# Kernel tuning notes

Hardware: AMD Instinct MI355X
Metric: run time of the kernel (lower is better)

The kernel has to match this reference:

```python
import jax, jax.numpy as jnp
import numpy as np

N = 50000      # nodes
E = 600000     # edges (avg degree 12)
IN, H, OUT = 128, 256, 256


def setup_inputs() -> dict:
    key = jax.random.key(0)
    ks = jax.random.split(key, 9)
    glorot = lambda k, shp: jax.random.uniform(
        k, shp, jnp.float32, -1.0, 1.0) * np.sqrt(6.0 / (shp[0] + shp[1]))
    return {
        "x": jax.random.normal(ks[0], (N, IN), jnp.float32),
        "src": jax.random.randint(ks[1], (E,), 0, N, jnp.int32),
        "dst": jax.random.randint(ks[2], (E,), 0, N, jnp.int32),
        "W_conv": glorot(ks[3], (IN, H)),
        "b_conv": jnp.zeros((H,), jnp.float32),
        "W_fc": glorot(ks[4], (H, H)),
        "b_fc": jax.random.uniform(ks[5], (H,), jnp.float32, -1, 1) / np.sqrt(H),
        "W_fc2": glorot(ks[6], (H, OUT)),
        "b_fc2": jax.random.uniform(ks[7], (OUT,), jnp.float32, -1, 1) / np.sqrt(OUT),
    }


def reference(x, src, dst, W_conv, b_conv, W_fc, b_fc, W_fc2, b_fc2):
    ones = jnp.ones((E,), x.dtype)
    # dgl GraphConv, norm='both': D_in^{-1/2} A D_out^{-1/2} X W + b
    deg_out = jax.ops.segment_sum(ones, src, num_segments=N)
    deg_in = jax.ops.segment_sum(ones, dst, num_segments=N)
    norm_src = jax.lax.rsqrt(jnp.maximum(deg_out, 1.0))  # [N]
    norm_dst = jax.lax.rsqrt(jnp.maximum(deg_in, 1.0))   # [N]
    feat = x * norm_src[:, None]                          # [N, IN]
    agg = jax.ops.segment_sum(feat[src], dst, num_segments=N)  # gather+scatter SpMM
    h = agg * norm_dst[:, None]
    h = h @ W_conv + b_conv                               # GraphConv weight+bias
    # num_nonl_layers == 2 branch
    h = jax.nn.relu(h) @ W_fc + b_fc
    h = jax.nn.relu(h) @ W_fc2 + b_fc2
    return h
```

## Files before the change

kernel.cpp:

```cpp
#include <hip/hip_runtime.h>

#define NN 50000
#define NE 600000
#define FIN 128
#define CAPS 128
#define CAPU 64
#define PW1 136
#define PW2 264

typedef __attribute__((ext_vector_type(8))) short bf16x8;
typedef __attribute__((ext_vector_type(4))) float f32x4;

__device__ __forceinline__ unsigned short f2bf(float f) {
    union { float f; unsigned int i; } v; v.f = f;
    return (unsigned short)((v.i + 0x7FFFu + ((v.i >> 16) & 1u)) >> 16);
}


__global__ __launch_bounds__(256)
void bin_kernel(const int* __restrict__ src, const int* __restrict__ dst,
                int* __restrict__ cnt_in, int* __restrict__ cnt_out,
                int* __restrict__ csr_src) {
    int e = blockIdx.x * 256 + threadIdx.x;
    if (e < NE) {
        int s = src[e], d = dst[e];
        int p = atomicAdd(&cnt_in[d], 1);
        if (p < CAPU) csr_src[d * CAPS + p] = s;
        atomicAdd(&cnt_out[s], 1);
    }
}

__global__ __launch_bounds__(256)
void gather_kernel(const float* __restrict__ x, const int* __restrict__ csr_src,
                   const int* __restrict__ cnt_in, const int* __restrict__ cnt_out,
                   char* __restrict__ slotbase) {
    int tid  = threadIdx.x;
    int grp  = tid >> 5;
    int lane = tid & 31;
    int r = blockIdx.x * 8 + grp;
    if (r >= NN) return;
    int deg = cnt_in[r];
    float nd = rsqrtf(fmaxf((float)deg, 1.0f));
    int cnt = deg > CAPU ? CAPU : deg;
    const int* bucket = csr_src + (size_t)r * CAPS;
    const float* xb = x + lane * 4;
    float4 acc = {0.f, 0.f, 0.f, 0.f};
    for (int j0 = 0; j0 < cnt; j0 += 32) {
        int c = cnt - j0; if (c > 32) c = 32;
        int sv = 0; float nsl = 0.f;
        if (lane < c) {
            sv  = bucket[j0 + lane];
            nsl = rsqrtf(fmaxf((float)cnt_out[sv], 1.0f));
        }
        int i = 0;
        for (; i + 4 <= c; i += 4) {
            int   s0 = __shfl(sv, i, 32),     s1 = __shfl(sv, i + 1, 32);
            int   s2 = __shfl(sv, i + 2, 32), s3 = __shfl(sv, i + 3, 32);
            float n0 = __shfl(nsl, i, 32),     n1 = __shfl(nsl, i + 1, 32);
            float n2 = __shfl(nsl, i + 2, 32), n3 = __shfl(nsl, i + 3, 32);
            float4 v0 = *(const float4*)(xb + (size_t)s0 * FIN);
            float4 v1 = *(const float4*)(xb + (size_t)s1 * FIN);
            float4 v2 = *(const float4*)(xb + (size_t)s2 * FIN);
            float4 v3 = *(const float4*)(xb + (size_t)s3 * FIN);
            acc.x += v0.x * n0; acc.y += v0.y * n0; acc.z += v0.z * n0; acc.w += v0.w * n0;
            acc.x += v1.x * n1; acc.y += v1.y * n1; acc.z += v1.z * n1; acc.w += v1.w * n1;
            acc.x += v2.x * n2; acc.y += v2.y * n2; acc.z += v2.z * n2; acc.w += v2.w * n2;
            acc.x += v3.x * n3; acc.y += v3.y * n3; acc.z += v3.z * n3; acc.w += v3.w * n3;
        }
        for (; i < c; ++i) {
            int   s  = __shfl(sv,  i, 32);
            float ns = __shfl(nsl, i, 32);
            float4 xv = *(const float4*)(xb + (size_t)s * FIN);
            acc.x += xv.x * ns; acc.y += xv.y * ns;
            acc.z += xv.z * ns; acc.w += xv.w * ns;
        }
    }
    unsigned short o[4];
    o[0] = f2bf(acc.x * nd); o[1] = f2bf(acc.y * nd);
    o[2] = f2bf(acc.z * nd); o[3] = f2bf(acc.w * nd);
    *(uint2*)(slotbase + (size_t)r * 1024 + 768 + lane * 8) = *(const uint2*)o;
}

__global__ __launch_bounds__(256)
void wprep_kernel(const float* __restrict__ Wc, const float* __restrict__ W1,
                  const float* __restrict__ W2, unsigned short* __restrict__ o) {
    int t = blockIdx.x * 256 + threadIdx.x;
    if (t < 32768) {
        int n = t >> 7, k = t & 127;
        o[t] = f2bf(Wc[k * 256 + n]);
    } else if (t < 98304) {
        int i = t - 32768; int n = i >> 8, k = i & 255;
        o[32768 + i] = f2bf(W1[k * 256 + n]);
    } else if (t < 163840) {
        int i = t - 98304; int n = i >> 8, k = i & 255;
        o[98304 + i] = f2bf(W2[k * 256 + n]);
    }
}

__global__ __launch_bounds__(256)
void gemm1_kernel(char* slotbase, const unsigned short* __restrict__ Wct,
                  const float* __restrict__ bc) {
    __shared__ short wsh[64 * PW1];
    int tid = threadIdx.x;
    int wave = tid >> 6, lane = tid & 63;
    int quad = lane >> 4, l16 = lane & 15;
    int m0 = blockIdx.x * 128 + wave * 32;
    bf16x8 a[2][4];
    #pragma unroll
    for (int g = 0; g < 2; ++g) {
        int arow = m0 + g * 16 + l16; if (arow >= NN) arow = NN - 1;
        const unsigned short* Ap =
            (const unsigned short*)(slotbase + (size_t)arow * 1024 + 768) + quad * 8;
        #pragma unroll
        for (int i = 0; i < 4; ++i) a[g][i] = *(const bf16x8*)(Ap + i * 32);
    }
    int sc = tid >> 2, sq = tid & 3;
    #pragma unroll 1
    for (int p = 0; p < 4; ++p) {
        __syncthreads();
        {
            const unsigned short* g = Wct + (size_t)(p * 64 + sc) * 128 + sq * 32;
            #pragma unroll
            for (int j = 0; j < 4; ++j)
                *(bf16x8*)&wsh[sc * PW1 + sq * 32 + j * 8] = *(const bf16x8*)(g + j * 8);
        }
        __syncthreads();
        f32x4 acc[2][4] = {};
        #pragma unroll
        for (int i = 0; i < 4; ++i) {
            int k0 = i * 32;
            bf16x8 b0 = *(const bf16x8*)&wsh[( 0 + l16) * PW1 + quad * 8 + k0];
            bf16x8 b1 = *(const bf16x8*)&wsh[(16 + l16) * PW1 + quad * 8 + k0];
            bf16x8 b2 = *(const bf16x8*)&wsh[(32 + l16) * PW1 + quad * 8 + k0];
            bf16x8 b3 = *(const bf16x8*)&wsh[(48 + l16) * PW1 + quad * 8 + k0];
            #pragma unroll
            for (int g = 0; g < 2; ++g) {
                acc[g][0] = __builtin_amdgcn_mfma_f32_16x16x32_bf16(a[g][i], b0, acc[g][0], 0, 0, 0);
                acc[g][1] = __builtin_amdgcn_mfma_f32_16x16x32_bf16(a[g][i], b1, acc[g][1], 0, 0, 0);
                acc[g][2] = __builtin_amdgcn_mfma_f32_16x16x32_bf16(a[g][i], b2, acc[g][2], 0, 0, 0);
                acc[g][3] = __builtin_amdgcn_mfma_f32_16x16x32_bf16(a[g][i], b3, acc[g][3], 0, 0, 0);
            }
        }
        int n0 = p * 64;
        #pragma unroll
        for (int c = 0; c < 4; ++c) {
            int col = n0 + c * 16 + l16;
            float bv = bc[col];
            #pragma unroll
            for (int g = 0; g < 2; ++g) {
                #pragma unroll
                for (int r2 = 0; r2 < 4; ++r2) {
                    int rr = m0 + g * 16 + quad * 4 + r2;
                    if (rr < NN)
                        *(unsigned short*)(slotbase + (size_t)rr * 1024 + 512 + 2 * col) =
                            f2bf(fmaxf(acc[g][c][r2] + bv, 0.0f));
                }
            }
        }
    }
}

template<bool FINAL>
__global__ __launch_bounds__(256)
void gemm23_kernel(char* slotbase, const unsigned short* __restrict__ Wt,
                   const float* __restrict__ bias) {
    __shared__ short wsh[64 * PW2];
    int tid = threadIdx.x;
    int wave = tid >> 6, lane = tid & 63;
    int quad = lane >> 4, l16 = lane & 15;
    int m0 = blockIdx.x * 128 + wave * 32;
    bf16x8 a[2][8];
    #pragma unroll
    for (int g = 0; g < 2; ++g) {
        int arow = m0 + g * 16 + l16; if (arow >= NN) arow = NN - 1;
        const unsigned short* Ap =
            (const unsigned short*)(slotbase + (size_t)arow * 1024 + (FINAL ? 0 : 512)) + quad * 8;
        #pragma unroll
        for (int i = 0; i < 8; ++i) a[g][i] = *(const bf16x8*)(Ap + i * 32);
    }
    int sc = tid >> 2, sq = tid & 3;
    #pragma unroll 1
    for (int p = 0; p < 4; ++p) {
        __syncthreads();
        {
            const unsigned short* g = Wt + (size_t)(p * 64 + sc) * 256 + sq * 64;
            #pragma unroll
            for (int j = 0; j < 8; ++j)
                *(bf16x8*)&wsh[sc * PW2 + sq * 64 + j * 8] = *(const bf16x8*)(g + j * 8);
        }
        __syncthreads();
        f32x4 acc[2][4] = {};
        #pragma unroll
        for (int i = 0; i < 8; ++i) {
            int k0 = i * 32;
            bf16x8 b0 = *(const bf16x8*)&wsh[( 0 + l16) * PW2 + quad * 8 + k0];
            bf16x8 b1 = *(const bf16x8*)&wsh[(16 + l16) * PW2 + quad * 8 + k0];
            bf16x8 b2 = *(const bf16x8*)&wsh[(32 + l16) * PW2 + quad * 8 + k0];
            bf16x8 b3 = *(const bf16x8*)&wsh[(48 + l16) * PW2 + quad * 8 + k0];
            #pragma unroll
            for (int g = 0; g < 2; ++g) {
                acc[g][0] = __builtin_amdgcn_mfma_f32_16x16x32_bf16(a[g][i], b0, acc[g][0], 0, 0, 0);
                acc[g][1] = __builtin_amdgcn_mfma_f32_16x16x32_bf16(a[g][i], b1, acc[g][1], 0, 0, 0);
                acc[g][2] = __builtin_amdgcn_mfma_f32_16x16x32_bf16(a[g][i], b2, acc[g][2], 0, 0, 0);
                acc[g][3] = __builtin_amdgcn_mfma_f32_16x16x32_bf16(a[g][i], b3, acc[g][3], 0, 0, 0);
            }
        }
        int n0 = p * 64;
        #pragma unroll
        for (int c = 0; c < 4; ++c) {
            int col = n0 + c * 16 + l16;
            float bv = bias[col];
            #pragma unroll
            for (int g = 0; g < 2; ++g) {
                #pragma unroll
                for (int r2 = 0; r2 < 4; ++r2) {
                    int rr = m0 + g * 16 + quad * 4 + r2;
                    if (rr < NN) {
                        float v = acc[g][c][r2] + bv;
                        if (FINAL)
                            *(float*)(slotbase + (size_t)rr * 1024 + 4 * col) = v;
                        else
                            *(unsigned short*)(slotbase + (size_t)rr * 1024 + 2 * col) =
                                f2bf(fmaxf(v, 0.0f));
                    }
                }
            }
        }
    }
}


extern "C" void kernel_launch(void* const* d_in, const int* in_sizes, int n_in,
                              void* d_out, int out_size, void* d_ws, size_t ws_size,
                              hipStream_t stream) {
    const float* x      = (const float*)d_in[0];
    const int*   src    = (const int*)d_in[1];
    const int*   dst    = (const int*)d_in[2];
    const float* W_conv = (const float*)d_in[3];
    const float* b_conv = (const float*)d_in[4];
    const float* W_fc   = (const float*)d_in[5];
    const float* b_fc   = (const float*)d_in[6];
    const float* W_fc2  = (const float*)d_in[7];
    const float* b_fc2  = (const float*)d_in[8];
    char* slotbase = (char*)d_out;

    int* csr_src = (int*)(slotbase + 16000000);

    char* ws = (char*)d_ws;
    int* cnt_out = (int*)(ws + 0);
    int* cnt_in  = (int*)(ws + 204800);
    unsigned short* Wct = (unsigned short*)(ws + 0);
    unsigned short* W1t = (unsigned short*)(ws + 65536);
    unsigned short* W2t = (unsigned short*)(ws + 196608);

    hipMemsetAsync(d_ws, 0, 409600, stream);

    bin_kernel<<<(NE + 255) / 256, 256, 0, stream>>>(src, dst, cnt_in, cnt_out,
                                                     csr_src);
    gather_kernel<<<(NN + 7) / 8, 256, 0, stream>>>(x, csr_src, cnt_in, cnt_out,
                                                    slotbase);
    wprep_kernel<<<640, 256, 0, stream>>>(W_conv, W_fc, W_fc2, (unsigned short*)ws);

    int nb = (NN + 127) / 128;
    gemm1_kernel<<<nb, 256, 0, stream>>>(slotbase, Wct, b_conv);
    gemm23_kernel<false><<<nb, 256, 0, stream>>>(slotbase, W1t, b_fc);
    gemm23_kernel<true ><<<nb, 256, 0, stream>>>(slotbase, W2t, b_fc2);
}
```

Baseline: 274.6 us.

## Split GEMM output columns across grid and shrink final GEMM row tile

The first two GEMMs now launch a second grid dimension, so each block computes 128 of the 256 output columns and the block count doubles. To let two blocks read the same input rows safely, the scratch-slot offsets change: gemm1 now writes to offset 0 and gemm2 writes to offset 512. The final GEMM uses a 64-row tile with one 16-row group per wave, which also gives more blocks. The aim is to fill more of the CUs, since about 391 blocks of 128 rows leaves many idle. The cost is that each input A tile is loaded twice, and the final layer has less register reuse.

```diff
diff --git a/kernel.cpp b/kernel.cpp
--- a/kernel.cpp
+++ b/kernel.cpp
@@ -116,10 +116,11 @@
     }
     int sc = tid >> 2, sq = tid & 3;
     #pragma unroll 1
-    for (int p = 0; p < 4; ++p) {
+    for (int p = 0; p < 2; ++p) {
+        int n0 = blockIdx.y * 128 + p * 64;
         __syncthreads();
         {
-            const unsigned short* g = Wct + (size_t)(p * 64 + sc) * 128 + sq * 32;
+            const unsigned short* g = Wct + (size_t)(n0 + sc) * 128 + sq * 32;
             #pragma unroll
             for (int j = 0; j < 4; ++j)
                 *(bf16x8*)&wsh[sc * PW1 + sq * 32 + j * 8] = *(const bf16x8*)(g + j * 8);
@@ -141,7 +142,6 @@
                 acc[g][3] = __builtin_amdgcn_mfma_f32_16x16x32_bf16(a[g][i], b3, acc[g][3], 0, 0, 0);
             }
         }
-        int n0 = p * 64;
         #pragma unroll
         for (int c = 0; c < 4; ++c) {
             int col = n0 + c * 16 + l16;
@@ -152,7 +152,7 @@
                 for (int r2 = 0; r2 < 4; ++r2) {
                     int rr = m0 + g * 16 + quad * 4 + r2;
                     if (rr < NN)
-                        *(unsigned short*)(slotbase + (size_t)rr * 1024 + 512 + 2 * col) =
+                        *(unsigned short*)(slotbase + (size_t)rr * 1024 + 2 * col) =
                             f2bf(fmaxf(acc[g][c][r2] + bv, 0.0f));
                 }
             }
@@ -160,10 +160,9 @@
     }
 }
 
-template<bool FINAL>
-__global__ __launch_bounds__(256)
-void gemm23_kernel(char* slotbase, const unsigned short* __restrict__ Wt,
-                   const float* __restrict__ bias) {
+__global__ __launch_bounds__(256)
+void gemm2_kernel(char* slotbase, const unsigned short* __restrict__ Wt,
+                  const float* __restrict__ bias) {
     __shared__ short wsh[64 * PW2];
     int tid = threadIdx.x;
     int wave = tid >> 6, lane = tid & 63;
@@ -174,16 +173,17 @@
     for (int g = 0; g < 2; ++g) {
         int arow = m0 + g * 16 + l16; if (arow >= NN) arow = NN - 1;
         const unsigned short* Ap =
-            (const unsigned short*)(slotbase + (size_t)arow * 1024 + (FINAL ? 0 : 512)) + quad * 8;
+            (const unsigned short*)(slotbase + (size_t)arow * 1024) + quad * 8;
         #pragma unroll
         for (int i = 0; i < 8; ++i) a[g][i] = *(const bf16x8*)(Ap + i * 32);
     }
     int sc = tid >> 2, sq = tid & 3;
     #pragma unroll 1
-    for (int p = 0; p < 4; ++p) {
+    for (int p = 0; p < 2; ++p) {
+        int n0 = blockIdx.y * 128 + p * 64;
         __syncthreads();
         {
-            const unsigned short* g = Wt + (size_t)(p * 64 + sc) * 256 + sq * 64;
+            const unsigned short* g = Wt + (size_t)(n0 + sc) * 256 + sq * 64;
             #pragma unroll
             for (int j = 0; j < 8; ++j)
                 *(bf16x8*)&wsh[sc * PW2 + sq * 64 + j * 8] = *(const bf16x8*)(g + j * 8);
@@ -205,7 +205,6 @@
                 acc[g][3] = __builtin_amdgcn_mfma_f32_16x16x32_bf16(a[g][i], b3, acc[g][3], 0, 0, 0);
             }
         }
-        int n0 = p * 64;
         #pragma unroll
         for (int c = 0; c < 4; ++c) {
             int col = n0 + c * 16 + l16;
@@ -215,15 +214,64 @@
                 #pragma unroll
                 for (int r2 = 0; r2 < 4; ++r2) {
                     int rr = m0 + g * 16 + quad * 4 + r2;
-                    if (rr < NN) {
-                        float v = acc[g][c][r2] + bv;
-                        if (FINAL)
-                            *(float*)(slotbase + (size_t)rr * 1024 + 4 * col) = v;
-                        else
-                            *(unsigned short*)(slotbase + (size_t)rr * 1024 + 2 * col) =
-                                f2bf(fmaxf(v, 0.0f));
-                    }
+                    if (rr < NN)
+                        *(unsigned short*)(slotbase + (size_t)rr * 1024 + 512 + 2 * col) =
+                            f2bf(fmaxf(acc[g][c][r2] + bv, 0.0f));
                 }
+            }
+        }
+    }
+}
+
+__global__ __launch_bounds__(256)
+void gemm3_kernel(char* slotbase, const unsigned short* __restrict__ Wt,
+                  const float* __restrict__ bias) {
+    __shared__ short wsh[64 * PW2];
+    int tid = threadIdx.x;
+    int wave = tid >> 6, lane = tid & 63;
+    int quad = lane >> 4, l16 = lane & 15;
+    int m0 = blockIdx.x * 64 + wave * 16;
+    int arow = m0 + l16; if (arow >= NN) arow = NN - 1;
+    const unsigned short* Ap =
+        (const unsigned short*)(slotbase + (size_t)arow * 1024 + 512) + quad * 8;
+    bf16x8 a[8];
+    #pragma unroll
+    for (int i = 0; i < 8; ++i) a[i] = *(const bf16x8*)(Ap + i * 32);
+    int sc = tid >> 2, sq = tid & 3;
+    #pragma unroll 1
+    for (int p = 0; p < 4; ++p) {
+        __syncthreads();
+        {
+            const unsigned short* g = Wt + (size_t)(p * 64 + sc) * 256 + sq * 64;
+            #pragma unroll
+            for (int j = 0; j < 8; ++j)
+                *(bf16x8*)&wsh[sc * PW2 + sq * 64 + j * 8] = *(const bf16x8*)(g + j * 8);
+        }
+        __syncthreads();
+        f32x4 ac0 = {0.f,0.f,0.f,0.f}, ac1 = ac0, ac2 = ac0, ac3 = ac0;
+        #pragma unroll
+        for (int i = 0; i < 8; ++i) {
+            int k0 = i * 32;
+            bf16x8 b0 = *(const bf16x8*)&wsh[( 0 + l16) * PW2 + quad * 8 + k0];
+            bf16x8 b1 = *(const bf16x8*)&wsh[(16 + l16) * PW2 + quad * 8 + k0];
+            bf16x8 b2 = *(const bf16x8*)&wsh[(32 + l16) * PW2 + quad * 8 + k0];
+            bf16x8 b3 = *(const bf16x8*)&wsh[(48 + l16) * PW2 + quad * 8 + k0];
+            ac0 = __builtin_amdgcn_mfma_f32_16x16x32_bf16(a[i], b0, ac0, 0, 0, 0);
+            ac1 = __builtin_amdgcn_mfma_f32_16x16x32_bf16(a[i], b1, ac1, 0, 0, 0);
+            ac2 = __builtin_amdgcn_mfma_f32_16x16x32_bf16(a[i], b2, ac2, 0, 0, 0);
+            ac3 = __builtin_amdgcn_mfma_f32_16x16x32_bf16(a[i], b3, ac3, 0, 0, 0);
+        }
+        int n0 = p * 64;
+        f32x4 accs[4] = {ac0, ac1, ac2, ac3};
+        #pragma unroll
+        for (int c = 0; c < 4; ++c) {
+            int col = n0 + c * 16 + l16;
+            float bv = bias[col];
+            #pragma unroll
+            for (int r2 = 0; r2 < 4; ++r2) {
+                int rr = m0 + quad * 4 + r2;
+                if (rr < NN)
+                    *(float*)(slotbase + (size_t)rr * 1024 + 4 * col) = accs[c][r2] + bv;
             }
         }
     }
@@ -261,8 +309,8 @@
                                                     slotbase);
     wprep_kernel<<<640, 256, 0, stream>>>(W_conv, W_fc, W_fc2, (unsigned short*)ws);
 
-    int nb = (NN + 127) / 128;
-    gemm1_kernel<<<nb, 256, 0, stream>>>(slotbase, Wct, b_conv);
-    gemm23_kernel<false><<<nb, 256, 0, stream>>>(slotbase, W1t, b_fc);
-    gemm23_kernel<true ><<<nb, 256, 0, stream>>>(slotbase, W2t, b_fc2);
-}
+    dim3 g12((NN + 127) / 128, 2);
+    gemm1_kernel<<<g12, 256, 0, stream>>>(slotbase, Wct, b_conv);
+    gemm2_kernel<<<g12, 256, 0, stream>>>(slotbase, W1t, b_fc);
+    gemm3_kernel<<<(NN + 63) / 64, 256, 0, stream>>>(slotbase, W2t, b_fc2);
+}
```

Result: no change. 271.4 us (-1.2%).
